# Kernel tuning notes

Measured on AMD Instinct MI355X. Metric: run time of the kernel, lower is better.

Reference implementation:

```python
import jax, jax.numpy as jnp
import numpy as np

EPS = 1e-12  # matches torch F.normalize eps


def _gradients(img):
    # forward differences along D, H, W with last slice zeroed (via zero-pad)
    dx = jnp.pad(img[:, :, 1:] - img[:, :, :-1], ((0, 0), (0, 0), (0, 1), (0, 0), (0, 0)))
    dy = jnp.pad(img[:, :, :, 1:] - img[:, :, :, :-1], ((0, 0), (0, 0), (0, 0), (0, 1), (0, 0)))
    dz = jnp.pad(img[:, :, :, :, 1:] - img[:, :, :, :, :-1], ((0, 0), (0, 0), (0, 0), (0, 0), (0, 1)))
    return dx, dy, dz


def _cos(f, t, axis):
    # cosine similarity along `axis` with torch-normalize eps semantics
    fn = f / jnp.maximum(jnp.linalg.norm(f, axis=axis, keepdims=True), EPS)
    tn = t / jnp.maximum(jnp.linalg.norm(t, axis=axis, keepdims=True), EPS)
    return jnp.sum(fn * tn, axis=axis)


def _sploss(f, t, ax_row, ax_col):
    # trace(norm_rows(F) @ norm_rows(T)^T) == sum of row cosine sims; same for cols.
    bc = f.shape[0] * f.shape[1]
    a = jnp.sum(_cos(f, t, ax_col)) / (f.shape[ax_row] * bc)
    b = jnp.sum(_cos(f, t, ax_row)) / (f.shape[ax_col] * bc)
    return -(a + b)


def setup_inputs() -> dict:
    key = jax.random.key(0)
    k1, k2 = jax.random.split(key)
    shape = (2, 1, 160, 160, 160)  # [B, C, D, H, W]
    fake = jax.random.normal(k1, shape, dtype=jnp.float32)
    true = jax.random.normal(k2, shape, dtype=jnp.float32)
    return {"fake": fake, "true": true}


def reference(fake, true):
    fx, fy, fz = _gradients(fake)
    tx, ty, tz = _gradients(true)
    # dim='x' slices are [H, W] -> rows axis 3, cols axis 4
    trace_x = _sploss(fx, tx, 3, 4)
    # dim='y' slices are [D, W] -> rows axis 2, cols axis 4
    trace_y = _sploss(fy, ty, 2, 4)
    # dim='z' slices are [D, H] -> rows axis 2, cols axis 3
    trace_z = _sploss(fz, tz, 2, 3)
    return (trace_x + trace_y + trace_z) / 3.0
```

## Files before the change

### kernel.cpp

```cpp
#include <hip/hip_runtime.h>
#include <math.h>

#define DD 160
#define HH 160
#define WW 160
#define NB 2
#define SLICE (HH * WW)
#define NV 51200
#define NVTOT (4 * NV)
#define W4 40
#define NTHR 320

static constexpr float EPS = 1e-12f;
static constexpr float SCALE = -1.0f / 960.0f;

#define ELEM(v, j) ((j) == 0 ? (v).x : ((j) == 1 ? (v).y : ((j) == 2 ? (v).z : (v).w)))

__global__ void zero_kernel(float* out) {
  if (threadIdx.x == 0) out[0] = 0.0f;
}

__global__ __launch_bounds__(NTHR) void kernelA(const float* __restrict__ f,
                                                const float* __restrict__ t,
                                                float* __restrict__ P,
                                                float* __restrict__ out,
                                                int nc, int rows_pc, int niter) {
  const int tid = threadIdx.x;
  const int l = tid % W4;
  const int g = tid / W4;
  const int w = 4 * l;
  const int hc = blockIdx.x % nc;
  const int bd = blockIdx.x / nc;
  const int d = bd % DD;
  const size_t base = (size_t)bd * SLICE;
  const float* fp = f + base;
  const float* tp = t + base;
  const int dstep = (d < DD - 1) ? SLICE : 0;
  const int wn = (w + 4 < WW) ? (w + 4) : (WW - 1);

  __shared__ float sd[8][W4][25];
  __shared__ float red[8][6];
  __shared__ float cpart[8];

  float ah[24];
#pragma unroll
  for (int c = 0; c < 24; ++c) ah[c] = 0.0f;
  float accCos = 0.0f;

  for (int it = 0; it < niter; ++it) {
    const int h = hc * rows_pc + it * 8 + g;
    const float* rf = fp + h * WW;
    const float* rt = tp + h * WW;
    const int hstep = (h < HH - 1) ? WW : 0;
    const float4 F0 = *(const float4*)(rf + w);
    const float4 T0 = *(const float4*)(rt + w);
    const float4 FD = *(const float4*)(rf + dstep + w);
    const float4 TD = *(const float4*)(rt + dstep + w);
    const float4 FH = *(const float4*)(rf + hstep + w);
    const float4 TH = *(const float4*)(rt + hstep + w);
    const float fz = rf[wn], tz = rt[wn];

    float xd = 0, xf = 0, xt = 0, yd = 0, yf = 0, yt = 0;
#pragma unroll
    for (int j = 0; j < 4; ++j) {
      const float f0 = ELEM(F0, j), t0 = ELEM(T0, j);
      const float gxf = ELEM(FD, j) - f0, gxt = ELEM(TD, j) - t0;
      const float gyf = ELEM(FH, j) - f0, gyt = ELEM(TH, j) - t0;
      const float fnx = (j < 3) ? ELEM(F0, (j + 1)) : fz;
      const float tnx = (j < 3) ? ELEM(T0, (j + 1)) : tz;
      const float gzf = fnx - f0, gzt = tnx - t0;
      xd += gxf * gxt; xf += gxf * gxf; xt += gxt * gxt;
      yd += gyf * gyt; yf += gyf * gyf; yt += gyt * gyt;
      ah[j * 6 + 0] += gxf * gxt; ah[j * 6 + 1] += gxf * gxf; ah[j * 6 + 2] += gxt * gxt;
      ah[j * 6 + 3] += gzf * gzt; ah[j * 6 + 4] += gzf * gzf; ah[j * 6 + 5] += gzt * gzt;
    }
    sd[g][l][0] = xd; sd[g][l][1] = xf; sd[g][l][2] = xt;
    sd[g][l][3] = yd; sd[g][l][4] = yf; sd[g][l][5] = yt;
    __syncthreads();
    if (tid < 48) {
      const int rr = tid / 6, c = tid % 6;
      float s = 0.0f;
#pragma unroll 8
      for (int ll = 0; ll < W4; ++ll) s += sd[rr][ll][c];
      red[rr][c] = s;
    }
    __syncthreads();
    if (tid < 8) {
      const float cx = red[tid][0] / (fmaxf(sqrtf(red[tid][1]), EPS) * fmaxf(sqrtf(red[tid][2]), EPS));
      const float cy = red[tid][3] / (fmaxf(sqrtf(red[tid][4]), EPS) * fmaxf(sqrtf(red[tid][5]), EPS));
      accCos += cx + cy;
    }
    __syncthreads();
  }

  if (tid < 8) cpart[tid] = accCos;
#pragma unroll
  for (int c = 0; c < 24; ++c) sd[g][l][c] = ah[c];
  __syncthreads();
  if (tid == 0) {
    float s = 0.0f;
#pragma unroll
    for (int i = 0; i < 8; ++i) s += cpart[i];
    atomicAdd(out, s * SCALE);
  }
  for (int task = tid; task < 960; task += NTHR) {
    const int ll = task / 24, c = task % 24;
    float s = 0.0f;
#pragma unroll
    for (int gg = 0; gg < 8; ++gg) s += sd[gg][ll][c];
    const int j = c / 6, cc = c % 6;
    const int wi = 4 * ll + j;
    const size_t vec = (cc < 3) ? (size_t)(bd * 160 + wi) : (size_t)(NV + bd * 160 + wi);
    P[((size_t)hc * NVTOT + vec) * 3 + (cc % 3)] = s;
  }
}

__global__ __launch_bounds__(NTHR) void kernelB(const float* __restrict__ f,
                                                const float* __restrict__ t,
                                                float* __restrict__ P,
                                                int nc, int rows_pc, int niter) {
  const int tid = threadIdx.x;
  const int l = tid % W4;
  const int g = tid / W4;
  const int w = 4 * l;
  const int dc = blockIdx.x % nc;
  const int bh = blockIdx.x / nc;
  const int b = bh / HH;
  const int h = bh % HH;
  const size_t base = (size_t)b * DD * SLICE + (size_t)h * WW;
  const float* fp = f + base;
  const float* tp = t + base;
  const int hstep = (h < HH - 1) ? WW : 0;
  const int wn = (w + 4 < WW) ? (w + 4) : (WW - 1);

  __shared__ float sd[8][W4][25];
  float ad[24];
#pragma unroll
  for (int c = 0; c < 24; ++c) ad[c] = 0.0f;

  for (int it = 0; it < niter; ++it) {
    const int dloc = dc * rows_pc + it * 8 + g;
    const float* rf = fp + (size_t)dloc * SLICE;
    const float* rt = tp + (size_t)dloc * SLICE;
    const float4 F0 = *(const float4*)(rf + w);
    const float4 T0 = *(const float4*)(rt + w);
    const float4 FH = *(const float4*)(rf + hstep + w);
    const float4 TH = *(const float4*)(rt + hstep + w);
    const float fz = rf[wn], tz = rt[wn];
#pragma unroll
    for (int j = 0; j < 4; ++j) {
      const float f0 = ELEM(F0, j), t0 = ELEM(T0, j);
      const float gyf = ELEM(FH, j) - f0, gyt = ELEM(TH, j) - t0;
      const float fnx = (j < 3) ? ELEM(F0, (j + 1)) : fz;
      const float tnx = (j < 3) ? ELEM(T0, (j + 1)) : tz;
      const float gzf = fnx - f0, gzt = tnx - t0;
      ad[j * 6 + 0] += gyf * gyt; ad[j * 6 + 1] += gyf * gyf; ad[j * 6 + 2] += gyt * gyt;
      ad[j * 6 + 3] += gzf * gzt; ad[j * 6 + 4] += gzf * gzf; ad[j * 6 + 5] += gzt * gzt;
    }
  }
#pragma unroll
  for (int c = 0; c < 24; ++c) sd[g][l][c] = ad[c];
  __syncthreads();
  for (int task = tid; task < 960; task += NTHR) {
    const int ll = task / 24, c = task % 24;
    float s = 0.0f;
#pragma unroll
    for (int gg = 0; gg < 8; ++gg) s += sd[gg][ll][c];
    const int j = c / 6, cc = c % 6;
    const int wi = 4 * ll + j;
    const size_t vec = (cc < 3) ? (size_t)(2 * NV + bh * 160 + wi) : (size_t)(3 * NV + bh * 160 + wi);
    P[((size_t)dc * NVTOT + vec) * 3 + (cc % 3)] = s;
  }
}

__global__ __launch_bounds__(256) void finalize_kernel(const float* __restrict__ P,
                                                       float* __restrict__ out, int nc) {
  const int v = blockIdx.x * 256 + threadIdx.x;
  float c = 0.0f;
  if (v < NVTOT) {
    float dot = 0.0f, ff = 0.0f, tt = 0.0f;
    for (int ch = 0; ch < nc; ++ch) {
      const size_t o = ((size_t)ch * NVTOT + v) * 3;
      dot += P[o]; ff += P[o + 1]; tt += P[o + 2];
    }
    c = dot / (fmaxf(sqrtf(ff), EPS) * fmaxf(sqrtf(tt), EPS));
  }
#pragma unroll
  for (int m = 32; m >= 1; m >>= 1) c += __shfl_xor(c, m);
  __shared__ float part[4];
  if ((threadIdx.x & 63) == 0) part[threadIdx.x >> 6] = c;
  __syncthreads();
  if (threadIdx.x == 0) atomicAdd(out, (part[0] + part[1] + part[2] + part[3]) * SCALE);
}

extern "C" void kernel_launch(void* const* d_in, const int* in_sizes, int n_in,
                              void* d_out, int out_size, void* d_ws, size_t ws_size,
                              hipStream_t stream) {
  const float* fk = (const float*)d_in[0];
  const float* tr = (const float*)d_in[1];
  float* out = (float*)d_out;
  float* P = (float*)d_ws;

  const size_t need5 = (size_t)5 * NVTOT * 3 * sizeof(float);
  const int nc = (ws_size >= need5) ? 5 : 2;
  const int rows_pc = 160 / nc;
  const int niter = rows_pc / 8;

  hipLaunchKernelGGL(zero_kernel, dim3(1), dim3(64), 0, stream, out);
  hipLaunchKernelGGL(kernelA, dim3(NB * DD * nc), dim3(NTHR), 0, stream, fk, tr, P, out, nc, rows_pc, niter);
  hipLaunchKernelGGL(kernelB, dim3(NB * HH * nc), dim3(NTHR), 0, stream, fk, tr, P, nc, rows_pc, niter);
  hipLaunchKernelGGL(finalize_kernel, dim3((NVTOT + 255) / 256), dim3(256), 0, stream, P, out, nc);
}
```

Before: 149.6 us.

## Merge slice-pass kernels into one interleaved launch with batched row reductions

```diff
diff --git a/kernel.cpp b/kernel.cpp
--- a/kernel.cpp
+++ b/kernel.cpp
@@ -8,7 +8,9 @@
 #define SLICE (HH * WW)
 #define NV 51200
 #define NVTOT (4 * NV)
-#define W4 40
+#define NC 5
+#define RPC 32
+#define NIT 4
 #define NTHR 320
 
 static constexpr float EPS = 1e-12f;
@@ -20,166 +22,158 @@
   if (threadIdx.x == 0) out[0] = 0.0f;
 }
 
-__global__ __launch_bounds__(NTHR) void kernelA(const float* __restrict__ f,
-                                                const float* __restrict__ t,
-                                                float* __restrict__ P,
-                                                float* __restrict__ out,
-                                                int nc, int rows_pc, int niter) {
+__global__ __launch_bounds__(NTHR) void mainAB(const float* __restrict__ f,
+                                               const float* __restrict__ t,
+                                               float* __restrict__ P,
+                                               float* __restrict__ out) {
+  __shared__ float sd[8960];
+  __shared__ float red[32][6];
+  __shared__ float cpad[32];
   const int tid = threadIdx.x;
-  const int l = tid % W4;
-  const int g = tid / W4;
+  const int l = tid % 40;
+  const int g = tid / 40;
   const int w = 4 * l;
-  const int hc = blockIdx.x % nc;
-  const int bd = blockIdx.x / nc;
-  const int d = bd % DD;
-  const size_t base = (size_t)bd * SLICE;
-  const float* fp = f + base;
-  const float* tp = t + base;
-  const int dstep = (d < DD - 1) ? SLICE : 0;
   const int wn = (w + 4 < WW) ? (w + 4) : (WW - 1);
-
-  __shared__ float sd[8][W4][25];
-  __shared__ float red[8][6];
-  __shared__ float cpart[8];
-
-  float ah[24];
-#pragma unroll
-  for (int c = 0; c < 24; ++c) ah[c] = 0.0f;
-  float accCos = 0.0f;
-
-  for (int it = 0; it < niter; ++it) {
-    const int h = hc * rows_pc + it * 8 + g;
-    const float* rf = fp + h * WW;
-    const float* rt = tp + h * WW;
-    const int hstep = (h < HH - 1) ? WW : 0;
-    const float4 F0 = *(const float4*)(rf + w);
-    const float4 T0 = *(const float4*)(rt + w);
-    const float4 FD = *(const float4*)(rf + dstep + w);
-    const float4 TD = *(const float4*)(rt + dstep + w);
-    const float4 FH = *(const float4*)(rf + hstep + w);
-    const float4 TH = *(const float4*)(rt + hstep + w);
-    const float fz = rf[wn], tz = rt[wn];
-
-    float xd = 0, xf = 0, xt = 0, yd = 0, yf = 0, yt = 0;
-#pragma unroll
-    for (int j = 0; j < 4; ++j) {
-      const float f0 = ELEM(F0, j), t0 = ELEM(T0, j);
-      const float gxf = ELEM(FD, j) - f0, gxt = ELEM(TD, j) - t0;
-      const float gyf = ELEM(FH, j) - f0, gyt = ELEM(TH, j) - t0;
-      const float fnx = (j < 3) ? ELEM(F0, (j + 1)) : fz;
-      const float tnx = (j < 3) ? ELEM(T0, (j + 1)) : tz;
-      const float gzf = fnx - f0, gzt = tnx - t0;
-      xd += gxf * gxt; xf += gxf * gxf; xt += gxt * gxt;
-      yd += gyf * gyt; yf += gyf * gyf; yt += gyt * gyt;
-      ah[j * 6 + 0] += gxf * gxt; ah[j * 6 + 1] += gxf * gxf; ah[j * 6 + 2] += gxt * gxt;
-      ah[j * 6 + 3] += gzf * gzt; ah[j * 6 + 4] += gzf * gzf; ah[j * 6 + 5] += gzt * gzt;
-    }
-    sd[g][l][0] = xd; sd[g][l][1] = xf; sd[g][l][2] = xt;
-    sd[g][l][3] = yd; sd[g][l][4] = yf; sd[g][l][5] = yt;
-    __syncthreads();
-    if (tid < 48) {
-      const int rr = tid / 6, c = tid % 6;
+  const int blk = blockIdx.x;
+
+  if ((blk & 1) == 0) {
+    const int id = blk >> 1;
+    const int hc = id % NC;
+    const int bd = id / NC;
+    const int d = bd % DD;
+    const size_t base = (size_t)bd * SLICE;
+    const float* fp = f + base;
+    const float* tp = t + base;
+    const int dstep = (d < DD - 1) ? SLICE : 0;
+    float ah[24];
+#pragma unroll
+    for (int c = 0; c < 24; ++c) ah[c] = 0.0f;
+
+#pragma unroll
+    for (int it = 0; it < NIT; ++it) {
+      const int rl = it * 8 + g;
+      const int h = hc * RPC + rl;
+      const int hstep = (h < HH - 1) ? WW : 0;
+      const float* rf = fp + h * WW;
+      const float* rt = tp + h * WW;
+      const float4 F0 = *(const float4*)(rf + w);
+      const float4 T0 = *(const float4*)(rt + w);
+      const float4 FD = *(const float4*)(rf + dstep + w);
+      const float4 TD = *(const float4*)(rt + dstep + w);
+      const float4 FH = *(const float4*)(rf + hstep + w);
+      const float4 TH = *(const float4*)(rt + hstep + w);
+      const float fz = rf[wn], tz = rt[wn];
+      float xd = 0, xf = 0, xt = 0, yd = 0, yf = 0, yt = 0;
+#pragma unroll
+      for (int j = 0; j < 4; ++j) {
+        const float f0 = ELEM(F0, j), t0 = ELEM(T0, j);
+        const float gxf = ELEM(FD, j) - f0, gxt = ELEM(TD, j) - t0;
+        const float gyf = ELEM(FH, j) - f0, gyt = ELEM(TH, j) - t0;
+        const float fnx = (j < 3) ? ELEM(F0, j + 1) : fz;
+        const float tnx = (j < 3) ? ELEM(T0, j + 1) : tz;
+        const float gzf = fnx - f0, gzt = tnx - t0;
+        xd += gxf * gxt; xf += gxf * gxf; xt += gxt * gxt;
+        yd += gyf * gyt; yf += gyf * gyf; yt += gyt * gyt;
+        ah[j * 6 + 0] += gxf * gxt; ah[j * 6 + 1] += gxf * gxf; ah[j * 6 + 2] += gxt * gxt;
+        ah[j * 6 + 3] += gzf * gzt; ah[j * 6 + 4] += gzf * gzf; ah[j * 6 + 5] += gzt * gzt;
+      }
+      float* s = &sd[(rl * 40 + l) * 7];
+      s[0] = xd; s[1] = xf; s[2] = xt; s[3] = yd; s[4] = yf; s[5] = yt;
+    }
+    __syncthreads();
+    if (tid < 192) {
+      const int row = tid / 6, c = tid % 6;
       float s = 0.0f;
 #pragma unroll 8
-      for (int ll = 0; ll < W4; ++ll) s += sd[rr][ll][c];
-      red[rr][c] = s;
-    }
-    __syncthreads();
-    if (tid < 8) {
+      for (int ll = 0; ll < 40; ++ll) s += sd[(row * 40 + ll) * 7 + c];
+      red[row][c] = s;
+    }
+    __syncthreads();
+    if (tid < 32) {
       const float cx = red[tid][0] / (fmaxf(sqrtf(red[tid][1]), EPS) * fmaxf(sqrtf(red[tid][2]), EPS));
       const float cy = red[tid][3] / (fmaxf(sqrtf(red[tid][4]), EPS) * fmaxf(sqrtf(red[tid][5]), EPS));
-      accCos += cx + cy;
-    }
-    __syncthreads();
+      cpad[tid] = cx + cy;
+    }
+    float* s3 = &sd[(g * 40 + l) * 25];
+#pragma unroll
+    for (int c = 0; c < 24; ++c) s3[c] = ah[c];
+    __syncthreads();
+    if (tid == 0) {
+      float s = 0.0f;
+#pragma unroll
+      for (int i = 0; i < 32; ++i) s += cpad[i];
+      atomicAdd(out, s * SCALE);
+    }
+    for (int task = tid; task < 960; task += NTHR) {
+      const int ll = task / 24, c = task % 24;
+      float s = 0.0f;
+#pragma unroll
+      for (int gg = 0; gg < 8; ++gg) s += sd[(gg * 40 + ll) * 25 + c];
+      const int j = c / 6, cc = c % 6;
+      const int wi = 4 * ll + j;
+      const size_t vec = (cc < 3) ? (size_t)(bd * 160 + wi) : (size_t)(NV + bd * 160 + wi);
+      P[((size_t)hc * NVTOT + vec) * 3 + (cc % 3)] = s;
+    }
+  } else {
+    const int id = blk >> 1;
+    const int dc = id % NC;
+    const int bh = id / NC;
+    const int b = bh / HH;
+    const int h = bh % HH;
+    const size_t base = (size_t)b * DD * SLICE + (size_t)h * WW;
+    const float* fp = f + base;
+    const float* tp = t + base;
+    const int hstep = (h < HH - 1) ? WW : 0;
+    float ad[24];
+#pragma unroll
+    for (int c = 0; c < 24; ++c) ad[c] = 0.0f;
+
+#pragma unroll
+    for (int it = 0; it < NIT; ++it) {
+      const int dloc = dc * RPC + it * 8 + g;
+      const float* rf = fp + (size_t)dloc * SLICE;
+      const float* rt = tp + (size_t)dloc * SLICE;
+      const float4 F0 = *(const float4*)(rf + w);
+      const float4 T0 = *(const float4*)(rt + w);
+      const float4 FH = *(const float4*)(rf + hstep + w);
+      const float4 TH = *(const float4*)(rt + hstep + w);
+      const float fz = rf[wn], tz = rt[wn];
+#pragma unroll
+      for (int j = 0; j < 4; ++j) {
+        const float f0 = ELEM(F0, j), t0 = ELEM(T0, j);
+        const float gyf = ELEM(FH, j) - f0, gyt = ELEM(TH, j) - t0;
+        const float fnx = (j < 3) ? ELEM(F0, j + 1) : fz;
+        const float tnx = (j < 3) ? ELEM(T0, j + 1) : tz;
+        const float gzf = fnx - f0, gzt = tnx - t0;
+        ad[j * 6 + 0] += gyf * gyt; ad[j * 6 + 1] += gyf * gyf; ad[j * 6 + 2] += gyt * gyt;
+        ad[j * 6 + 3] += gzf * gzt; ad[j * 6 + 4] += gzf * gzf; ad[j * 6 + 5] += gzt * gzt;
+      }
+    }
+    float* s3 = &sd[(g * 40 + l) * 25];
+#pragma unroll
+    for (int c = 0; c < 24; ++c) s3[c] = ad[c];
+    __syncthreads();
+    for (int task = tid; task < 960; task += NTHR) {
+      const int ll = task / 24, c = task % 24;
+      float s = 0.0f;
+#pragma unroll
+      for (int gg = 0; gg < 8; ++gg) s += sd[(gg * 40 + ll) * 25 + c];
+      const int j = c / 6, cc = c % 6;
+      const int wi = 4 * ll + j;
+      const size_t vec = (cc < 3) ? (size_t)(2 * NV + bh * 160 + wi) : (size_t)(3 * NV + bh * 160 + wi);
+      P[((size_t)dc * NVTOT + vec) * 3 + (cc % 3)] = s;
+    }
   }
-
-  if (tid < 8) cpart[tid] = accCos;
-#pragma unroll
-  for (int c = 0; c < 24; ++c) sd[g][l][c] = ah[c];
-  __syncthreads();
-  if (tid == 0) {
-    float s = 0.0f;
-#pragma unroll
-    for (int i = 0; i < 8; ++i) s += cpart[i];
-    atomicAdd(out, s * SCALE);
-  }
-  for (int task = tid; task < 960; task += NTHR) {
-    const int ll = task / 24, c = task % 24;
-    float s = 0.0f;
-#pragma unroll
-    for (int gg = 0; gg < 8; ++gg) s += sd[gg][ll][c];
-    const int j = c / 6, cc = c % 6;
-    const int wi = 4 * ll + j;
-    const size_t vec = (cc < 3) ? (size_t)(bd * 160 + wi) : (size_t)(NV + bd * 160 + wi);
-    P[((size_t)hc * NVTOT + vec) * 3 + (cc % 3)] = s;
-  }
-}
-
-__global__ __launch_bounds__(NTHR) void kernelB(const float* __restrict__ f,
-                                                const float* __restrict__ t,
-                                                float* __restrict__ P,
-                                                int nc, int rows_pc, int niter) {
-  const int tid = threadIdx.x;
-  const int l = tid % W4;
-  const int g = tid / W4;
-  const int w = 4 * l;
-  const int dc = blockIdx.x % nc;
-  const int bh = blockIdx.x / nc;
-  const int b = bh / HH;
-  const int h = bh % HH;
-  const size_t base = (size_t)b * DD * SLICE + (size_t)h * WW;
-  const float* fp = f + base;
-  const float* tp = t + base;
-  const int hstep = (h < HH - 1) ? WW : 0;
-  const int wn = (w + 4 < WW) ? (w + 4) : (WW - 1);
-
-  __shared__ float sd[8][W4][25];
-  float ad[24];
-#pragma unroll
-  for (int c = 0; c < 24; ++c) ad[c] = 0.0f;
-
-  for (int it = 0; it < niter; ++it) {
-    const int dloc = dc * rows_pc + it * 8 + g;
-    const float* rf = fp + (size_t)dloc * SLICE;
-    const float* rt = tp + (size_t)dloc * SLICE;
-    const float4 F0 = *(const float4*)(rf + w);
-    const float4 T0 = *(const float4*)(rt + w);
-    const float4 FH = *(const float4*)(rf + hstep + w);
-    const float4 TH = *(const float4*)(rt + hstep + w);
-    const float fz = rf[wn], tz = rt[wn];
-#pragma unroll
-    for (int j = 0; j < 4; ++j) {
-      const float f0 = ELEM(F0, j), t0 = ELEM(T0, j);
-      const float gyf = ELEM(FH, j) - f0, gyt = ELEM(TH, j) - t0;
-      const float fnx = (j < 3) ? ELEM(F0, (j + 1)) : fz;
-      const float tnx = (j < 3) ? ELEM(T0, (j + 1)) : tz;
-      const float gzf = fnx - f0, gzt = tnx - t0;
-      ad[j * 6 + 0] += gyf * gyt; ad[j * 6 + 1] += gyf * gyf; ad[j * 6 + 2] += gyt * gyt;
-      ad[j * 6 + 3] += gzf * gzt; ad[j * 6 + 4] += gzf * gzf; ad[j * 6 + 5] += gzt * gzt;
-    }
-  }
-#pragma unroll
-  for (int c = 0; c < 24; ++c) sd[g][l][c] = ad[c];
-  __syncthreads();
-  for (int task = tid; task < 960; task += NTHR) {
-    const int ll = task / 24, c = task % 24;
-    float s = 0.0f;
-#pragma unroll
-    for (int gg = 0; gg < 8; ++gg) s += sd[gg][ll][c];
-    const int j = c / 6, cc = c % 6;
-    const int wi = 4 * ll + j;
-    const size_t vec = (cc < 3) ? (size_t)(2 * NV + bh * 160 + wi) : (size_t)(3 * NV + bh * 160 + wi);
-    P[((size_t)dc * NVTOT + vec) * 3 + (cc % 3)] = s;
-  }
 }
 
 __global__ __launch_bounds__(256) void finalize_kernel(const float* __restrict__ P,
-                                                       float* __restrict__ out, int nc) {
+                                                       float* __restrict__ out) {
   const int v = blockIdx.x * 256 + threadIdx.x;
   float c = 0.0f;
   if (v < NVTOT) {
     float dot = 0.0f, ff = 0.0f, tt = 0.0f;
-    for (int ch = 0; ch < nc; ++ch) {
+#pragma unroll
+    for (int ch = 0; ch < NC; ++ch) {
       const size_t o = ((size_t)ch * NVTOT + v) * 3;
       dot += P[o]; ff += P[o + 1]; tt += P[o + 2];
     }
@@ -201,13 +195,7 @@
   float* out = (float*)d_out;
   float* P = (float*)d_ws;
 
-  const size_t need5 = (size_t)5 * NVTOT * 3 * sizeof(float);
-  const int nc = (ws_size >= need5) ? 5 : 2;
-  const int rows_pc = 160 / nc;
-  const int niter = rows_pc / 8;
-
   hipLaunchKernelGGL(zero_kernel, dim3(1), dim3(64), 0, stream, out);
-  hipLaunchKernelGGL(kernelA, dim3(NB * DD * nc), dim3(NTHR), 0, stream, fk, tr, P, out, nc, rows_pc, niter);
-  hipLaunchKernelGGL(kernelB, dim3(NB * HH * nc), dim3(NTHR), 0, stream, fk, tr, P, nc, rows_pc, niter);
-  hipLaunchKernelGGL(finalize_kernel, dim3((NVTOT + 255) / 256), dim3(256), 0, stream, P, out, nc);
-}
+  hipLaunchKernelGGL(mainAB, dim3(2 * NB * DD * NC), dim3(NTHR), 0, stream, fk, tr, P, out);
+  hipLaunchKernelGGL(finalize_kernel, dim3((NVTOT + 255) / 256), dim3(256), 0, stream, P, out);
+}
```

Result: no change. 151.6 us (+1.3%).
